# Optimization experiments

Measured on AMD Instinct MI355X. Metric: run time of the kernel, lower is better.

The kernel has to match this reference:

```python
import jax, jax.numpy as jnp
import numpy as np

DIM = 1024
NUM_HEADS = 16
DIM_PER_HEAD = 64
INNER = NUM_HEADS * DIM_PER_HEAD  # 1024
SCALE = DIM_PER_HEAD ** -0.5
EPS = 1e-10


def setup_inputs() -> dict:
    key = jax.random.key(0)
    k_x, k_m, k_qkv, k_wo, k_bo = jax.random.split(key, 5)
    b, l = 2, 2048
    x = jax.random.normal(k_x, (b, l, DIM), dtype=jnp.float32)
    # binary multiplicative mask [b, l, l]
    mask = jax.random.randint(k_m, (b, l, l), 0, 2).astype(jnp.float32)
    # nn.Linear(dim, 3*inner, bias=False): weight [3*inner, dim]; we store transposed [dim, 3*inner]
    W_qkv = jax.random.normal(k_qkv, (DIM, 3 * INNER), dtype=jnp.float32) * (DIM ** -0.5)
    W_out = jax.random.normal(k_wo, (INNER, DIM), dtype=jnp.float32) * (INNER ** -0.5)
    b_out = jax.random.normal(k_bo, (DIM,), dtype=jnp.float32) * 0.01
    return {"x": x, "mask": mask, "W_qkv": W_qkv, "W_out": W_out, "b_out": b_out}


def reference(x, mask, W_qkv, W_out, b_out):
    b, l, d = x.shape
    qkv = x @ W_qkv  # [b, l, 3*inner]
    qkv = qkv.reshape(b, l, 3, NUM_HEADS, DIM_PER_HEAD)
    qkv = jnp.transpose(qkv, (2, 0, 3, 1, 4))  # [3, b, h, l, dh]
    q, k, v = qkv[0], qkv[1], qkv[2]
    # softmax FIRST (no additive mask), matching the original module
    attn = jax.nn.softmax(jnp.einsum('bhid,bhjd->bhij', q, k) * SCALE, axis=-1)  # [b,h,l,l]
    # multiplicative mask then renormalize
    attn = attn * mask[:, None, :, :]
    attn = attn / (jnp.sum(attn, axis=-1, keepdims=True) + EPS)
    z = jnp.einsum('bhij,bhjd->bhid', attn, v)  # [b,h,l,dh]
    z = jnp.transpose(z, (0, 2, 1, 3)).reshape(b, l, INNER)
    out = z @ W_out + b_out  # dropout p=0 -> identity
    return out
```

## Files before the change

### kernel.cpp

```cpp
#include <hip/hip_runtime.h>
#include <hip/hip_bf16.h>

#define BATCH 2
#define SEQ   2048
#define DIM   1024
#define HEADS 16
#define DH    64
#define N_QKV 3072
#define M_TOT 4096
#define SCALE 0.125f
#define EPS   1e-10f
#define LOG2E 1.442695041f

typedef __attribute__((ext_vector_type(8))) _Float16 half8;
typedef __attribute__((ext_vector_type(2))) _Float16 half2_t;
typedef __attribute__((ext_vector_type(4))) float f32x4;

static __device__ __forceinline__ unsigned short f2h(float f) {
    _Float16 h = (_Float16)f;
    return __builtin_bit_cast(unsigned short, h);
}
static __device__ __forceinline__ unsigned int pkrtz(float a, float b) {
#if defined(__has_builtin) && __has_builtin(__builtin_amdgcn_cvt_pkrtz)
    return __builtin_bit_cast(unsigned int, __builtin_amdgcn_cvt_pkrtz(a, b));
#else
    return (unsigned int)f2h(a) | ((unsigned int)f2h(b) << 16);
#endif
}
static __device__ __forceinline__ void glds16(const void* g, void* l) {
    __builtin_amdgcn_global_load_lds((const __attribute__((address_space(1))) void*)g,
                                     (__attribute__((address_space(3))) void*)l,
                                     16, 0, 0);
}

__global__ __launch_bounds__(256) void convert_f16(const float* __restrict__ s,
                                                   unsigned short* __restrict__ h) {
    const int i = blockIdx.x * 256 + threadIdx.x;
    float4 v = reinterpret_cast<const float4*>(s)[i];
    uint2 o;
    o.x = pkrtz(v.x, v.y);
    o.y = pkrtz(v.z, v.w);
    reinterpret_cast<uint2*>(h)[i] = o;
}

__global__ __launch_bounds__(256) void transpose_f16(const float* __restrict__ src,
                                                     unsigned short* __restrict__ th,
                                                     int rows, int cols) {
    __shared__ float tile[32][33];
    const int c0 = blockIdx.x * 32, r0 = blockIdx.y * 32;
    const int tx = threadIdx.x & 31, ty = threadIdx.x >> 5;
    #pragma unroll
    for (int i = ty; i < 32; i += 8)
        tile[i][tx] = src[(long)(r0 + i) * cols + c0 + tx];
    __syncthreads();
    #pragma unroll
    for (int i = ty; i < 32; i += 8)
        th[(long)(c0 + i) * rows + r0 + tx] = f2h(tile[tx][i]);
}

__global__ __launch_bounds__(256) void pack_maskbits(const float* __restrict__ mask,
                                                     unsigned short* __restrict__ mbits) {
    const int it = blockIdx.x;
    const int bb = blockIdx.y;
    const int t  = threadIdx.x;
    __shared__ unsigned char flags[16][256];
    const int R0 = it * 16;
    const int tl = t >> 6, ln = t & 63;

    for (int c0 = 0; c0 < SEQ; c0 += 256) {
        #pragma unroll
        for (int rr = 0; rr < 16; ++rr)
            flags[rr][t] = mask[((long)bb * SEQ + R0 + rr) * SEQ + c0 + t] != 0.f;
        __syncthreads();
        unsigned int bits = 0;
        #pragma unroll
        for (int nt = 0; nt < 4; ++nt)
            #pragma unroll
            for (int r = 0; r < 4; ++r)
                bits |= (unsigned int)flags[ln & 15][tl * 64 + nt * 16 + ((ln >> 4) << 2) + r]
                        << (nt * 4 + r);
        mbits[(((long)bb * 128 + it) * 32 + (c0 >> 6) + tl) * 64 + ln] = (unsigned short)bits;
        __syncthreads();
    }
}

__global__ __launch_bounds__(256) void gemm_qkv_f16(
    const unsigned short* __restrict__ Ahg, const unsigned short* __restrict__ Bhg,
    unsigned short* __restrict__ qb, unsigned short* __restrict__ kb,
    unsigned short* __restrict__ vtb) {
    __shared__ __align__(16) unsigned short As[128 * 64];
    __shared__ __align__(16) unsigned short Bs[128 * 64];

    const int n0   = blockIdx.x * 128;
    const int m0   = blockIdx.y * 128;
    const int wave = threadIdx.x >> 6;
    const int lane = threadIdx.x & 63;
    const int l16  = lane & 15;
    const int g    = lane >> 4;
    const int wm   = wave & 1;
    const int wn   = wave >> 1;
    const int sw   = l16 & 7;

    const int sr8 = lane >> 3;
    const int scg = (lane & 7) ^ sr8;

    f32x4 acc[4][4] = {};

    for (int k0 = 0; k0 < DIM; k0 += 64) {
        #pragma unroll
        for (int i = 0; i < 4; ++i) {
            const int row = wave * 32 + i * 8;
            glds16(Ahg + (long)(m0 + row + sr8) * DIM + k0 + scg * 8, &As[row * 64]);
            glds16(Bhg + (long)(n0 + row + sr8) * DIM + k0 + scg * 8, &Bs[row * 64]);
        }
        __syncthreads();

        half8 a[4][2];
        #pragma unroll
        for (int mt = 0; mt < 4; ++mt) {
            const int rbase = (wm * 64 + mt * 16 + l16) * 64;
            #pragma unroll
            for (int kc = 0; kc < 2; ++kc)
                a[mt][kc] = *reinterpret_cast<const half8*>(
                    &As[rbase + (((kc * 4 + g) ^ sw) * 8)]);
        }
        #pragma unroll
        for (int nt = 0; nt < 4; ++nt) {
            const int rbase = (wn * 64 + nt * 16 + l16) * 64;
            const half8 b0 = *reinterpret_cast<const half8*>(&Bs[rbase + (((0 + g) ^ sw) * 8)]);
            const half8 b1 = *reinterpret_cast<const half8*>(&Bs[rbase + (((4 + g) ^ sw) * 8)]);
            #pragma unroll
            for (int mt = 0; mt < 4; ++mt) {
                acc[mt][nt] = __builtin_amdgcn_mfma_f32_16x16x32_f16(a[mt][0], b0, acc[mt][nt], 0, 0, 0);
                acc[mt][nt] = __builtin_amdgcn_mfma_f32_16x16x32_f16(a[mt][1], b1, acc[mt][nt], 0, 0, 0);
            }
        }
        __syncthreads();
    }

    #pragma unroll
    for (int nt = 0; nt < 4; ++nt) {
        const int n     = n0 + wn * 64 + nt * 16 + l16;
        const int which = n >> 10;
        const int rem   = n & 1023;
        const int head  = rem >> 6;
        const int d     = rem & 63;
        #pragma unroll
        for (int mt = 0; mt < 4; ++mt) {
            #pragma unroll
            for (int r = 0; r < 4; ++r) {
                const int m  = m0 + wm * 64 + mt * 16 + g * 4 + r;
                const int bb = m >> 11;
                const int li = m & 2047;
                const int bh_i = bb * HEADS + head;
                const float val = acc[mt][nt][r];
                if (which == 0)
                    qb[((long)bh_i * SEQ + li) * DH + d] = f2h(val * SCALE);
                else if (which == 1)
                    kb[((long)bh_i * SEQ + li) * DH + d] = f2h(val);
                else
                    vtb[((long)bh_i * DH + d) * SEQ + li] = f2h(val);
            }
        }
    }
}

__global__ __launch_bounds__(256) void gemm_out_f16(
    const unsigned short* __restrict__ Ahg, const unsigned short* __restrict__ Bhg,
    const float* __restrict__ bias, float* __restrict__ out) {
    __shared__ __align__(16) unsigned short As[128 * 64];
    __shared__ __align__(16) unsigned short Bs[64 * 64];

    const int n0   = blockIdx.x * 64;
    const int m0   = blockIdx.y * 128;
    const int wave = threadIdx.x >> 6;
    const int lane = threadIdx.x & 63;
    const int l16  = lane & 15;
    const int g    = lane >> 4;
    const int sw   = l16 & 7;

    const int sr8 = lane >> 3;
    const int scg = (lane & 7) ^ sr8;

    f32x4 acc[2][4] = {};

    for (int k0 = 0; k0 < DIM; k0 += 64) {
        #pragma unroll
        for (int i = 0; i < 4; ++i) {
            const int row = wave * 32 + i * 8;
            glds16(Ahg + (long)(m0 + row + sr8) * DIM + k0 + scg * 8, &As[row * 64]);
        }
        #pragma unroll
        for (int i = 0; i < 2; ++i) {
            const int row = wave * 16 + i * 8;
            glds16(Bhg + (long)(n0 + row + sr8) * DIM + k0 + scg * 8, &Bs[row * 64]);
        }
        __syncthreads();

        half8 a[2][2];
        #pragma unroll
        for (int mt = 0; mt < 2; ++mt) {
            const int rbase = (wave * 32 + mt * 16 + l16) * 64;
            #pragma unroll
            for (int kc = 0; kc < 2; ++kc)
                a[mt][kc] = *reinterpret_cast<const half8*>(
                    &As[rbase + (((kc * 4 + g) ^ sw) * 8)]);
        }
        #pragma unroll
        for (int nt = 0; nt < 4; ++nt) {
            const int rbase = (nt * 16 + l16) * 64;
            const half8 b0 = *reinterpret_cast<const half8*>(&Bs[rbase + (((0 + g) ^ sw) * 8)]);
            const half8 b1 = *reinterpret_cast<const half8*>(&Bs[rbase + (((4 + g) ^ sw) * 8)]);
            #pragma unroll
            for (int mt = 0; mt < 2; ++mt) {
                acc[mt][nt] = __builtin_amdgcn_mfma_f32_16x16x32_f16(a[mt][0], b0, acc[mt][nt], 0, 0, 0);
                acc[mt][nt] = __builtin_amdgcn_mfma_f32_16x16x32_f16(a[mt][1], b1, acc[mt][nt], 0, 0, 0);
            }
        }
        __syncthreads();
    }

    #pragma unroll
    for (int nt = 0; nt < 4; ++nt) {
        const int n  = n0 + nt * 16 + l16;
        const float bv = bias[n];
        #pragma unroll
        for (int mt = 0; mt < 2; ++mt) {
            #pragma unroll
            for (int r = 0; r < 4; ++r) {
                const int m = m0 + wave * 32 + mt * 16 + g * 4 + r;
                out[(long)m * DIM + n] = acc[mt][nt][r] + bv;
            }
        }
    }
}

__global__ __launch_bounds__(512, 6) void attn_mfma(const unsigned short* __restrict__ qb,
                                                    const unsigned short* __restrict__ kb,
                                                    const unsigned short* __restrict__ vtb,
                                                    const unsigned short* __restrict__ mbits,
                                                    unsigned short* __restrict__ zh) {
    const int qt   = blockIdx.x;
    const int h    = blockIdx.y;
    const int bb   = blockIdx.z;
    const int bh   = bb * HEADS + h;
    const int wave = threadIdx.x >> 6;
    const int lane = threadIdx.x & 63;
    const int l16  = lane & 15;
    const int g    = lane >> 4;
    const int wm   = wave >> 1;
    const int wj   = wave & 1;

    const int myrow0 = qt * 64 + wm * 16;

    __shared__ __align__(16) unsigned short KV[2][2][64 * 64];
    __shared__ __align__(16) unsigned short Ps[8][16 * 64];

    const int sr8 = lane >> 3;
    const int scg = (lane & 7) ^ sr8;
    const int sw  = l16 & 7;

    const unsigned short* qptr = qb + ((long)bh * SEQ + myrow0 + l16) * DH + g * 8;
    const half8 q0 = *reinterpret_cast<const half8*>(qptr);
    const half8 q1 = *reinterpret_cast<const half8*>(qptr + 32);

    half8 ones;
    #pragma unroll
    for (int j = 0; j < 8; ++j) ones[j] = (_Float16)1.0f;

    f32x4 o[4] = {};
    f32x4 oz = {0.f, 0.f, 0.f, 0.f};
    const float C0 = 4.0f * LOG2E;

    const unsigned short* mb =
        mbits + (((long)bb * 128 + qt * 4 + wm) * 32 + wj * 16) * 64 + lane;
    const long kbase = (long)bh * SEQ * DH;
    const long vbase = (long)bh * DH * SEQ;
    const int  jb    = wj * 1024;

    for (int it = 0; it < 16; ++it) {
        const int j0 = jb + it * 64;
        const unsigned int bits = mb[(long)it * 64];

        #pragma unroll
        for (int i = 0; i < 2; ++i) {
            const int row = wm * 16 + i * 8;
            glds16(kb  + kbase + (long)(j0 + row + sr8) * DH + scg * 8, &KV[wj][0][row * 64]);
            glds16(vtb + vbase + (long)(row + sr8) * SEQ + j0 + scg * 8, &KV[wj][1][row * 64]);
        }
        __syncthreads();

        f32x4 st[4];
        #pragma unroll
        for (int nt = 0; nt < 4; ++nt) {
            const int rbase = (nt * 16 + l16) * 64;
            const half8 k0 = *reinterpret_cast<const half8*>(&KV[wj][0][rbase + ((0 + g) ^ sw) * 8]);
            const half8 k1 = *reinterpret_cast<const half8*>(&KV[wj][0][rbase + ((4 + g) ^ sw) * 8]);
            f32x4 acc = {0.f, 0.f, 0.f, 0.f};
            acc = __builtin_amdgcn_mfma_f32_16x16x32_f16(k0, q0, acc, 0, 0, 0);
            acc = __builtin_amdgcn_mfma_f32_16x16x32_f16(k1, q1, acc, 0, 0, 0);
            st[nt] = acc;
        }

        #pragma unroll
        for (int nt = 0; nt < 4; ++nt) {
            float pm[4];
            #pragma unroll
            for (int r = 0; r < 4; ++r) {
                const float p = __builtin_amdgcn_exp2f(fmaf(st[nt][r], LOG2E, -C0));
                pm[r] = ((bits >> (nt * 4 + r)) & 1u) ? p : 0.f;
            }
            uint2 pk;
            pk.x = pkrtz(pm[0], pm[1]);
            pk.y = pkrtz(pm[2], pm[3]);
            *reinterpret_cast<uint2*>(
                &Ps[wave][l16 * 64 + (((2 * nt + (g >> 1)) ^ sw) * 8) + (g & 1) * 4]) = pk;
        }

        const half8 pb0 = *reinterpret_cast<const half8*>(&Ps[wave][l16 * 64 + ((0 + g) ^ sw) * 8]);
        const half8 pb1 = *reinterpret_cast<const half8*>(&Ps[wave][l16 * 64 + ((4 + g) ^ sw) * 8]);
        #pragma unroll
        for (int dt = 0; dt < 4; ++dt) {
            const int vb = (dt * 16 + l16) * 64;
            const half8 v0 = *reinterpret_cast<const half8*>(&KV[wj][1][vb + ((0 + g) ^ sw) * 8]);
            const half8 v1 = *reinterpret_cast<const half8*>(&KV[wj][1][vb + ((4 + g) ^ sw) * 8]);
            o[dt] = __builtin_amdgcn_mfma_f32_16x16x32_f16(v0, pb0, o[dt], 0, 0, 0);
            o[dt] = __builtin_amdgcn_mfma_f32_16x16x32_f16(v1, pb1, o[dt], 0, 0, 0);
        }
        oz = __builtin_amdgcn_mfma_f32_16x16x32_f16(ones, pb0, oz, 0, 0, 0);
        oz = __builtin_amdgcn_mfma_f32_16x16x32_f16(ones, pb1, oz, 0, 0, 0);
        __syncthreads();
    }

    float* cmb = (float*)&KV[0][0][0];
    const int ci = wm * 16 + l16;
    if (wj == 1) {
        #pragma unroll
        for (int dt = 0; dt < 4; ++dt)
            *reinterpret_cast<f32x4*>(&cmb[ci * 68 + dt * 16 + g * 4]) = o[dt];
        if (g == 0) cmb[4352 + ci] = oz[0];
    }
    __syncthreads();
    if (wj == 0) {
        const float Z   = oz[0] + cmb[4352 + ci];
        const float inv = 1.f / (Z + 1e-30f);
        const long obase = ((long)bb * SEQ + myrow0 + l16) * DIM + h * DH;
        #pragma unroll
        for (int dt = 0; dt < 4; ++dt) {
            const f32x4 oc = *reinterpret_cast<const f32x4*>(&cmb[ci * 68 + dt * 16 + g * 4]);
            uint2 pk;
            pk.x = pkrtz((o[dt][0] + oc[0]) * inv, (o[dt][1] + oc[1]) * inv);
            pk.y = pkrtz((o[dt][2] + oc[2]) * inv, (o[dt][3] + oc[3]) * inv);
            *reinterpret_cast<uint2*>(zh + obase + dt * 16 + g * 4) = pk;
        }
    }
}

extern "C" void kernel_launch(void* const* d_in, const int* in_sizes, int n_in,
                              void* d_out, int out_size, void* d_ws, size_t ws_size,
                              hipStream_t stream) {
    const float* x     = (const float*)d_in[0];
    const float* mask  = (const float*)d_in[1];
    const float* W_qkv = (const float*)d_in[2];
    const float* W_out = (const float*)d_in[3];
    const float* b_out = (const float*)d_in[4];
    float* out = (float*)d_out;

    unsigned short* ws = (unsigned short*)d_ws;
    unsigned short* xh    = ws;
    unsigned short* WqT   = xh    + 4194304;
    unsigned short* WoT   = WqT   + 3145728;
    unsigned short* qb    = WoT   + 1048576;
    unsigned short* kb    = qb    + 4194304;
    unsigned short* vtb   = kb    + 4194304;
    unsigned short* mbits = vtb   + 4194304;
    unsigned short* zz    = xh;

    convert_f16<<<4096, 256, 0, stream>>>(x, xh);
    transpose_f16<<<dim3(96, 32), 256, 0, stream>>>(W_qkv, WqT, 1024, 3072);
    transpose_f16<<<dim3(32, 32), 256, 0, stream>>>(W_out, WoT, 1024, 1024);
    pack_maskbits<<<dim3(128, 2), 256, 0, stream>>>(mask, mbits);

    gemm_qkv_f16<<<dim3(24, 32), 256, 0, stream>>>(xh, WqT, qb, kb, vtb);

    attn_mfma<<<dim3(SEQ / 64, HEADS, BATCH), 512, 0, stream>>>(qb, kb, vtb, mbits, zz);

    gemm_out_f16<<<dim3(16, 32), 256, 0, stream>>>(zz, WoT, b_out, out);
}
```

Before: 248.3 us.

## Restructure attention so each wave owns a key slice for all 64 queries

The attention kernel drops from 512 to 256 threads. Each of four waves now processes all 64 query rows over its own quarter of the keys, using private LDS K/V/P buffers and a waitcnt instead of block-wide barriers inside the loop. Row sums are accumulated in registers instead of with an extra ones-MFMA, and partial outputs are reduced across waves through LDS at the end. The mask packing is reorganised into 32-bit words matching the new layout. The aim is to increase K/V reuse per load and remove per-iteration syncs, at the cost of more accumulator registers, lower pack_maskbits parallelism and a larger end-of-kernel reduction.

```diff
diff --git a/kernel.cpp b/kernel.cpp
--- a/kernel.cpp
+++ b/kernel.cpp
@@ -13,7 +13,6 @@
 #define LOG2E 1.442695041f
 
 typedef __attribute__((ext_vector_type(8))) _Float16 half8;
-typedef __attribute__((ext_vector_type(2))) _Float16 half2_t;
 typedef __attribute__((ext_vector_type(4))) float f32x4;
 
 static __device__ __forceinline__ unsigned short f2h(float f) {
@@ -59,27 +58,35 @@
 }
 
 __global__ __launch_bounds__(256) void pack_maskbits(const float* __restrict__ mask,
-                                                     unsigned short* __restrict__ mbits) {
-    const int it = blockIdx.x;
+                                                     unsigned int* __restrict__ mbits) {
+    const int qb = blockIdx.x;
     const int bb = blockIdx.y;
     const int t  = threadIdx.x;
-    __shared__ unsigned char flags[16][256];
-    const int R0 = it * 16;
-    const int tl = t >> 6, ln = t & 63;
+    __shared__ unsigned char flags[64][256];
 
     for (int c0 = 0; c0 < SEQ; c0 += 256) {
-        #pragma unroll
-        for (int rr = 0; rr < 16; ++rr)
-            flags[rr][t] = mask[((long)bb * SEQ + R0 + rr) * SEQ + c0 + t] != 0.f;
-        __syncthreads();
-        unsigned int bits = 0;
-        #pragma unroll
-        for (int nt = 0; nt < 4; ++nt)
-            #pragma unroll
-            for (int r = 0; r < 4; ++r)
-                bits |= (unsigned int)flags[ln & 15][tl * 64 + nt * 16 + ((ln >> 4) << 2) + r]
-                        << (nt * 4 + r);
-        mbits[(((long)bb * 128 + it) * 32 + (c0 >> 6) + tl) * 64 + ln] = (unsigned short)bits;
+        #pragma unroll 4
+        for (int rr = 0; rr < 64; ++rr)
+            flags[rr][t] = mask[((long)bb * SEQ + qb * 64 + rr) * SEQ + c0 + t] != 0.f;
+        __syncthreads();
+        #pragma unroll
+        for (int i = 0; i < 2; ++i) {
+            const int idx = i * 256 + t;
+            const int kg = idx >> 6;
+            const int ln = idx & 63;
+            const int lq = ln & 15, lg = ln >> 4;
+            unsigned int bits = 0;
+            #pragma unroll
+            for (int kt = 0; kt < 2; ++kt)
+                #pragma unroll
+                for (int qt = 0; qt < 4; ++qt)
+                    #pragma unroll
+                    for (int r = 0; r < 4; ++r)
+                        bits |= (unsigned int)
+                                flags[qt * 16 + lq][kg * 32 + kt * 16 + lg * 4 + r]
+                                << (kt * 16 + qt * 4 + r);
+            mbits[(((long)bb * 32 + qb) * 64 + (c0 >> 5) + kg) * 64 + ln] = bits;
+        }
         __syncthreads();
     }
 }
@@ -235,12 +242,11 @@
     }
 }
 
-__global__ __launch_bounds__(512, 6) void attn_mfma(const unsigned short* __restrict__ qb,
-                                                    const unsigned short* __restrict__ kb,
-                                                    const unsigned short* __restrict__ vtb,
-                                                    const unsigned short* __restrict__ mbits,
-                                                    unsigned short* __restrict__ zh) {
-    const int qt   = blockIdx.x;
+__global__ __launch_bounds__(256, 3) void attn_mfma(
+    const unsigned short* __restrict__ qb, const unsigned short* __restrict__ kb,
+    const unsigned short* __restrict__ vtb, const unsigned int* __restrict__ mbits,
+    unsigned short* __restrict__ zz) {
+    const int qblk = blockIdx.x;
     const int h    = blockIdx.y;
     const int bb   = blockIdx.z;
     const int bh   = bb * HEADS + h;
@@ -248,111 +254,132 @@
     const int lane = threadIdx.x & 63;
     const int l16  = lane & 15;
     const int g    = lane >> 4;
-    const int wm   = wave >> 1;
-    const int wj   = wave & 1;
-
-    const int myrow0 = qt * 64 + wm * 16;
-
-    __shared__ __align__(16) unsigned short KV[2][2][64 * 64];
-    __shared__ __align__(16) unsigned short Ps[8][16 * 64];
-
-    const int sr8 = lane >> 3;
-    const int scg = (lane & 7) ^ sr8;
-    const int sw  = l16 & 7;
-
-    const unsigned short* qptr = qb + ((long)bh * SEQ + myrow0 + l16) * DH + g * 8;
-    const half8 q0 = *reinterpret_cast<const half8*>(qptr);
-    const half8 q1 = *reinterpret_cast<const half8*>(qptr + 32);
-
-    half8 ones;
-    #pragma unroll
-    for (int j = 0; j < 8; ++j) ones[j] = (_Float16)1.0f;
-
-    f32x4 o[4] = {};
-    f32x4 oz = {0.f, 0.f, 0.f, 0.f};
+    const int q0r  = qblk * 64;
+
+    __shared__ __align__(16) unsigned short SMEM[4][6144];
+    __shared__ float Zs[4][4][16];
+
+    unsigned short* myK = &SMEM[wave][0];
+    unsigned short* myV = &SMEM[wave][2048];
+    unsigned short* myP = &SMEM[wave][4096];
+
+    const int sw8 = l16 & 7;
+    const int swv = (l16 >> 1) & 3;
+    const int skr = lane >> 3;
+    const int skc = ((lane & 7) ^ skr) * 8;
+    const int svr = lane >> 2;
+    const int svc = ((lane & 3) ^ ((svr >> 1) & 3)) * 8;
+
+    half8 qf[4][2];
+    #pragma unroll
+    for (int qt = 0; qt < 4; ++qt) {
+        const unsigned short* qp = qb + ((long)bh * SEQ + q0r + qt * 16 + l16) * DH + g * 8;
+        qf[qt][0] = *reinterpret_cast<const half8*>(qp);
+        qf[qt][1] = *reinterpret_cast<const half8*>(qp + 32);
+    }
+
+    f32x4 o[4][4] = {};
+    float Zq[4] = {0.f, 0.f, 0.f, 0.f};
     const float C0 = 4.0f * LOG2E;
 
-    const unsigned short* mb =
-        mbits + (((long)bb * 128 + qt * 4 + wm) * 32 + wj * 16) * 64 + lane;
+    const unsigned int* mb = mbits + (((long)bb * 32 + qblk) * 64 + wave * 16) * 64 + lane;
     const long kbase = (long)bh * SEQ * DH;
     const long vbase = (long)bh * DH * SEQ;
-    const int  jb    = wj * 1024;
+    const int  jb    = wave * 512;
 
     for (int it = 0; it < 16; ++it) {
-        const int j0 = jb + it * 64;
-        const unsigned int bits = mb[(long)it * 64];
-
-        #pragma unroll
-        for (int i = 0; i < 2; ++i) {
-            const int row = wm * 16 + i * 8;
-            glds16(kb  + kbase + (long)(j0 + row + sr8) * DH + scg * 8, &KV[wj][0][row * 64]);
-            glds16(vtb + vbase + (long)(row + sr8) * SEQ + j0 + scg * 8, &KV[wj][1][row * 64]);
-        }
-        __syncthreads();
-
-        f32x4 st[4];
-        #pragma unroll
-        for (int nt = 0; nt < 4; ++nt) {
-            const int rbase = (nt * 16 + l16) * 64;
-            const half8 k0 = *reinterpret_cast<const half8*>(&KV[wj][0][rbase + ((0 + g) ^ sw) * 8]);
-            const half8 k1 = *reinterpret_cast<const half8*>(&KV[wj][0][rbase + ((4 + g) ^ sw) * 8]);
-            f32x4 acc = {0.f, 0.f, 0.f, 0.f};
-            acc = __builtin_amdgcn_mfma_f32_16x16x32_f16(k0, q0, acc, 0, 0, 0);
-            acc = __builtin_amdgcn_mfma_f32_16x16x32_f16(k1, q1, acc, 0, 0, 0);
-            st[nt] = acc;
-        }
-
-        #pragma unroll
-        for (int nt = 0; nt < 4; ++nt) {
-            float pm[4];
-            #pragma unroll
-            for (int r = 0; r < 4; ++r) {
-                const float p = __builtin_amdgcn_exp2f(fmaf(st[nt][r], LOG2E, -C0));
-                pm[r] = ((bits >> (nt * 4 + r)) & 1u) ? p : 0.f;
-            }
-            uint2 pk;
-            pk.x = pkrtz(pm[0], pm[1]);
-            pk.y = pkrtz(pm[2], pm[3]);
-            *reinterpret_cast<uint2*>(
-                &Ps[wave][l16 * 64 + (((2 * nt + (g >> 1)) ^ sw) * 8) + (g & 1) * 4]) = pk;
-        }
-
-        const half8 pb0 = *reinterpret_cast<const half8*>(&Ps[wave][l16 * 64 + ((0 + g) ^ sw) * 8]);
-        const half8 pb1 = *reinterpret_cast<const half8*>(&Ps[wave][l16 * 64 + ((4 + g) ^ sw) * 8]);
-        #pragma unroll
-        for (int dt = 0; dt < 4; ++dt) {
-            const int vb = (dt * 16 + l16) * 64;
-            const half8 v0 = *reinterpret_cast<const half8*>(&KV[wj][1][vb + ((0 + g) ^ sw) * 8]);
-            const half8 v1 = *reinterpret_cast<const half8*>(&KV[wj][1][vb + ((4 + g) ^ sw) * 8]);
-            o[dt] = __builtin_amdgcn_mfma_f32_16x16x32_f16(v0, pb0, o[dt], 0, 0, 0);
-            o[dt] = __builtin_amdgcn_mfma_f32_16x16x32_f16(v1, pb1, o[dt], 0, 0, 0);
-        }
-        oz = __builtin_amdgcn_mfma_f32_16x16x32_f16(ones, pb0, oz, 0, 0, 0);
-        oz = __builtin_amdgcn_mfma_f32_16x16x32_f16(ones, pb1, oz, 0, 0, 0);
-        __syncthreads();
-    }
-
-    float* cmb = (float*)&KV[0][0][0];
-    const int ci = wm * 16 + l16;
-    if (wj == 1) {
+        const int j0 = jb + it * 32;
+        const unsigned int bits = mb[it * 64];
+
+        #pragma unroll
+        for (int i = 0; i < 4; ++i)
+            glds16(kb + kbase + (long)(j0 + i * 8 + skr) * DH + skc, myK + i * 512);
+        #pragma unroll
+        for (int i = 0; i < 4; ++i)
+            glds16(vtb + vbase + (long)(i * 16 + svr) * SEQ + j0 + svc, myV + i * 512);
+        __builtin_amdgcn_s_waitcnt(0x0F70);
+
+        #pragma unroll
+        for (int kt = 0; kt < 2; ++kt) {
+            const int rb = (kt * 16 + l16) * 64;
+            const half8 k0 = *reinterpret_cast<const half8*>(&myK[rb + ((g ^ sw8) * 8)]);
+            const half8 k1 = *reinterpret_cast<const half8*>(&myK[rb + (((4 + g) ^ sw8) * 8)]);
+            f32x4 st[4];
+            #pragma unroll
+            for (int qt = 0; qt < 4; ++qt) {
+                f32x4 acc = {0.f, 0.f, 0.f, 0.f};
+                acc = __builtin_amdgcn_mfma_f32_16x16x32_f16(k0, qf[qt][0], acc, 0, 0, 0);
+                acc = __builtin_amdgcn_mfma_f32_16x16x32_f16(k1, qf[qt][1], acc, 0, 0, 0);
+                st[qt] = acc;
+            }
+            #pragma unroll
+            for (int qt = 0; qt < 4; ++qt) {
+                float pm[4];
+                #pragma unroll
+                for (int r = 0; r < 4; ++r) {
+                    const float p = __builtin_amdgcn_exp2f(fmaf(st[qt][r], LOG2E, -C0));
+                    pm[r] = ((bits >> (kt * 16 + qt * 4 + r)) & 1u) ? p : 0.f;
+                }
+                Zq[qt] += (pm[0] + pm[1]) + (pm[2] + pm[3]);
+                uint2 pk2;
+                pk2.x = pkrtz(pm[0], pm[1]);
+                pk2.y = pkrtz(pm[2], pm[3]);
+                *reinterpret_cast<uint2*>(&myP[(qt * 16 + l16) * 32 + kt * 16 + g * 4]) = pk2;
+            }
+        }
+
+        half8 va[4];
         #pragma unroll
         for (int dt = 0; dt < 4; ++dt)
-            *reinterpret_cast<f32x4*>(&cmb[ci * 68 + dt * 16 + g * 4]) = o[dt];
-        if (g == 0) cmb[4352 + ci] = oz[0];
-    }
+            va[dt] = *reinterpret_cast<const half8*>(&myV[(dt * 16 + l16) * 32 + ((g ^ swv) * 8)]);
+        #pragma unroll
+        for (int qt = 0; qt < 4; ++qt) {
+            const half8 pbq = *reinterpret_cast<const half8*>(&myP[(qt * 16 + l16) * 32 + g * 8]);
+            #pragma unroll
+            for (int dt = 0; dt < 4; ++dt)
+                o[dt][qt] = __builtin_amdgcn_mfma_f32_16x16x32_f16(va[dt], pbq, o[dt][qt], 0, 0, 0);
+        }
+    }
+
+    #pragma unroll
+    for (int qt = 0; qt < 4; ++qt) {
+        Zq[qt] += __shfl_xor(Zq[qt], 16, 64);
+        Zq[qt] += __shfl_xor(Zq[qt], 32, 64);
+    }
+
     __syncthreads();
-    if (wj == 0) {
-        const float Z   = oz[0] + cmb[4352 + ci];
-        const float inv = 1.f / (Z + 1e-30f);
-        const long obase = ((long)bb * SEQ + myrow0 + l16) * DIM + h * DH;
-        #pragma unroll
-        for (int dt = 0; dt < 4; ++dt) {
-            const f32x4 oc = *reinterpret_cast<const f32x4*>(&cmb[ci * 68 + dt * 16 + g * 4]);
-            uint2 pk;
-            pk.x = pkrtz((o[dt][0] + oc[0]) * inv, (o[dt][1] + oc[1]) * inv);
-            pk.y = pkrtz((o[dt][2] + oc[2]) * inv, (o[dt][3] + oc[3]) * inv);
-            *reinterpret_cast<uint2*>(zh + obase + dt * 16 + g * 4) = pk;
-        }
+    float* lx = (float*)&SMEM[0][0];
+    #pragma unroll
+    for (int dt = 0; dt < 4; ++dt) {
+        if (dt == wave) continue;
+        const int up = (wave < dt) ? wave : wave - 1;
+        #pragma unroll
+        for (int qt = 0; qt < 4; ++qt)
+            *reinterpret_cast<f32x4*>(&lx[((dt * 3 + up) * 4 + qt) * 256 + lane * 4]) = o[dt][qt];
+    }
+    if (g == 0) {
+        #pragma unroll
+        for (int qt = 0; qt < 4; ++qt) Zs[wave][qt][l16] = Zq[qt];
+    }
+    __syncthreads();
+
+    const int dto = wave;
+    #pragma unroll
+    for (int qt = 0; qt < 4; ++qt) {
+        const float Zt = Zs[0][qt][l16] + Zs[1][qt][l16] + Zs[2][qt][l16] + Zs[3][qt][l16];
+        const float inv = 1.f / (Zt + 1e-30f);
+        f32x4 acc = o[dto][qt];
+        #pragma unroll
+        for (int up = 0; up < 3; ++up) {
+            const f32x4 p = *reinterpret_cast<const f32x4*>(
+                &lx[((dto * 3 + up) * 4 + qt) * 256 + lane * 4]);
+            acc[0] += p[0]; acc[1] += p[1]; acc[2] += p[2]; acc[3] += p[3];
+        }
+        uint2 pk2;
+        pk2.x = pkrtz(acc[0] * inv, acc[1] * inv);
+        pk2.y = pkrtz(acc[2] * inv, acc[3] * inv);
+        const long addr = ((long)bb * SEQ + q0r + qt * 16 + l16) * DIM + h * DH + dto * 16 + g * 4;
+        *reinterpret_cast<uint2*>(&zz[addr]) = pk2;
     }
 }
 
@@ -367,23 +394,23 @@
     float* out = (float*)d_out;
 
     unsigned short* ws = (unsigned short*)d_ws;
-    unsigned short* xh    = ws;
-    unsigned short* WqT   = xh    + 4194304;
-    unsigned short* WoT   = WqT   + 3145728;
-    unsigned short* qb    = WoT   + 1048576;
-    unsigned short* kb    = qb    + 4194304;
-    unsigned short* vtb   = kb    + 4194304;
-    unsigned short* mbits = vtb   + 4194304;
-    unsigned short* zz    = xh;
+    unsigned short* xh  = ws;
+    unsigned short* WqT = xh  + 4194304;
+    unsigned short* WoT = WqT + 3145728;
+    unsigned short* qbu = WoT + 1048576;
+    unsigned short* kbu = qbu + 4194304;
+    unsigned short* vtb = kbu + 4194304;
+    unsigned int*   mbits = (unsigned int*)(vtb + 4194304);
+    unsigned short* zz  = xh;
 
     convert_f16<<<4096, 256, 0, stream>>>(x, xh);
     transpose_f16<<<dim3(96, 32), 256, 0, stream>>>(W_qkv, WqT, 1024, 3072);
     transpose_f16<<<dim3(32, 32), 256, 0, stream>>>(W_out, WoT, 1024, 1024);
-    pack_maskbits<<<dim3(128, 2), 256, 0, stream>>>(mask, mbits);
-
-    gemm_qkv_f16<<<dim3(24, 32), 256, 0, stream>>>(xh, WqT, qb, kb, vtb);
-
-    attn_mfma<<<dim3(SEQ / 64, HEADS, BATCH), 512, 0, stream>>>(qb, kb, vtb, mbits, zz);
+    pack_maskbits<<<dim3(32, 2), 256, 0, stream>>>(mask, mbits);
+
+    gemm_qkv_f16<<<dim3(24, 32), 256, 0, stream>>>(xh, WqT, qbu, kbu, vtb);
+
+    attn_mfma<<<dim3(SEQ / 64, HEADS, BATCH), 256, 0, stream>>>(qbu, kbu, vtb, mbits, zz);
 
     gemm_out_f16<<<dim3(16, 32), 256, 0, stream>>>(zz, WoT, b_out, out);
 }
```

Result: slower. 322.5 us (+29.9%).
